# Kernel tuning notes

Measured on AMD Instinct MI355X. Metric: run time of the kernel, lower is better.

The kernel has to match this reference:

```python
import jax, jax.numpy as jnp
import numpy as np

EPS = 1e-5  # BatchNorm eps (torch default)

def setup_inputs() -> dict:
    key = jax.random.key(0)
    ks = jax.random.split(key, 24)
    B, NX, NY, F = 8, 128, 128, 128
    dims = [2 * F, 512, 256, 128, 64]
    d = {
        'x': jax.random.normal(ks[0], (B, NX, F), dtype=jnp.float32),
        'y': jax.random.normal(ks[1], (B, NY, F), dtype=jnp.float32),
    }
    i = 2
    for li, (din, dout) in enumerate(zip(dims[:-1], dims[1:]), start=1):
        d[f'w{li}'] = jax.random.normal(ks[i], (dout, din), dtype=jnp.float32) * (1.0 / np.sqrt(din)); i += 1
        d[f'b{li}'] = jax.random.normal(ks[i], (dout,), dtype=jnp.float32) * 0.02; i += 1
        if li < 4:  # BatchNorm1d on hidden layers only (eval mode: running stats)
            d[f'g{li}'] = 1.0 + 0.1 * jax.random.normal(ks[i], (dout,), dtype=jnp.float32); i += 1
            d[f'be{li}'] = 0.1 * jax.random.normal(ks[i], (dout,), dtype=jnp.float32); i += 1
            d[f'm{li}'] = 0.1 * jax.random.normal(ks[i], (dout,), dtype=jnp.float32); i += 1
            d[f'v{li}'] = 0.5 + jax.random.uniform(ks[i], (dout,), dtype=jnp.float32); i += 1
    return d

def _bn(h, g, be, m, v):
    # BatchNorm1d in eval mode over the channel (last) axis
    return (h - m) * (g * jax.lax.rsqrt(v + EPS)) + be

def reference(x, y,
              w1, b1, g1, be1, m1, v1,
              w2, b2, g2, be2, m2, v2,
              w3, b3, g3, be3, m3, v3,
              w4, b4):
    F = x.shape[-1]
    # First Linear on cat([x_i, y_j]) == split-weight broadcast add: avoids the
    # (B,nx,ny,2F) pairwise concat the torch code materializes (same math).
    wx, wy = w1[:, :F], w1[:, F:]                      # (512,F) each
    hx = jnp.einsum('bif,hf->bih', x, wx)              # (B,nx,512)
    hy = jnp.einsum('bjf,hf->bjh', y, wy)              # (B,ny,512)
    h = hx[:, :, None, :] + hy[:, None, :, :] + b1     # (B,nx,ny,512)
    h = jax.nn.relu(_bn(h, g1, be1, m1, v1))           # dropout is identity in eval
    h = jax.nn.relu(_bn(jnp.einsum('bijh,oh->bijo', h, w2) + b2, g2, be2, m2, v2))
    h = jax.nn.relu(_bn(jnp.einsum('bijh,oh->bijo', h, w3) + b3, g3, be3, m3, v3))
    e = jnp.einsum('bijh,oh->bijo', h, w4) + b4        # (B,nx,ny,64) embeddings
    # PSD path: einsum('bijk,bilk->bijl', e, e).sum(-1)
    #         == sum_k e[b,i,j,k] * (sum_l e[b,i,l,k])  -- avoids (B,nx,ny,ny)
    s = e.sum(axis=2)                                  # (B,nx,64)
    kernel = jnp.einsum('bijk,bik->bij', e, s)         # (B,nx,ny)
    return kernel
```

## Files before the change

kernel.cpp:

```cpp
#include <hip/hip_runtime.h>

#define EPS 1e-5f

typedef _Float16 half8 __attribute__((ext_vector_type(8)));
typedef _Float16 half4 __attribute__((ext_vector_type(4)));
typedef float f32x16 __attribute__((ext_vector_type(16)));
typedef float f32x4v __attribute__((ext_vector_type(4)));


__global__ __launch_bounds__(256)
void pre_kernel(
    const float* __restrict__ x, const float* __restrict__ y,
    const float* __restrict__ w1, const float* __restrict__ b1,
    const float* __restrict__ g1, const float* __restrict__ be1,
    const float* __restrict__ m1, const float* __restrict__ v1,
    const float* __restrict__ w2, const float* __restrict__ b2,
    const float* __restrict__ g2, const float* __restrict__ be2,
    const float* __restrict__ m2, const float* __restrict__ v2,
    const float* __restrict__ w3, const float* __restrict__ b3,
    const float* __restrict__ g3, const float* __restrict__ be3,
    const float* __restrict__ m3, const float* __restrict__ v3,
    const float* __restrict__ w4,
    _Float16* __restrict__ hxh, _Float16* __restrict__ hyh,
    _Float16* __restrict__ w2h, _Float16* __restrict__ w3h,
    _Float16* __restrict__ w4h,
    float* __restrict__ b2f, float* __restrict__ b3f)
{
    const int t = threadIdx.x;

    if (blockIdx.x >= 256) {
        int tid = (blockIdx.x - 256) * 256 + t;
        const int nth = 64 * 256;
        for (int idx = tid; idx < 256 * 512; idx += nth) {
            int n = idx >> 9, k = idx & 511;
            float a = g2[n] * rsqrtf(v2[n] + EPS);
            int addr = ((n >> 5) * 32 + (k >> 4)) * 512 + ((k >> 3) & 1) * 256 + (n & 31) * 8 + (k & 7);
            w2h[addr] = (_Float16)(a * w2[idx]);
        }
        for (int idx = tid; idx < 128 * 256; idx += nth) {
            int n = idx >> 8, k = idx & 255;
            float a = g3[n] * rsqrtf(v3[n] + EPS);
            int addr = ((n >> 5) * 16 + (k >> 4)) * 512 + ((k >> 3) & 1) * 256 + (n & 31) * 8 + (k & 7);
            w3h[addr] = (_Float16)(a * w3[idx]);
        }
        for (int idx = tid; idx < 64 * 128; idx += nth) {
            int n = idx >> 7, k = idx & 127;
            int addr = ((n >> 5) * 8 + (k >> 4)) * 512 + ((k >> 3) & 1) * 256 + (n & 31) * 8 + (k & 7);
            w4h[addr] = (_Float16)w4[idx];
        }
        if (tid < 256) {
            float a = g2[tid] * rsqrtf(v2[tid] + EPS);
            b2f[tid] = a * b2[tid] + be2[tid] - m2[tid] * a;
        } else if (tid < 384) {
            int n = tid - 256;
            float a = g3[n] * rsqrtf(v3[n] + EPS);
            b3f[n] = a * b3[n] + be3[n] - m3[n] * a;
        }
        return;
    }

    const int rg = blockIdx.x & 31;
    const int ng = (blockIdx.x >> 5) & 3;
    const int which = blockIdx.x >> 7;

    constexpr int LDA = 136;
    __shared__ _Float16 sh[32 * 136 + 128 * 136] __attribute__((aligned(16)));
    _Float16* xa = sh;
    _Float16* wb = sh + 32 * 136;

    const int rowbase = rg * 32;
    const float* src = which ? y : x;

#pragma unroll
    for (int p = 0; p < 4; ++p) {
        int c = p * 256 + t;
        int r = c >> 5, fo = (c & 31) * 4;
        f32x4v v = *(const f32x4v*)(src + (size_t)(rowbase + r) * 128 + fo);
        half4 h; h[0] = (_Float16)v[0]; h[1] = (_Float16)v[1];
        h[2] = (_Float16)v[2]; h[3] = (_Float16)v[3];
        *(half4*)(xa + r * LDA + fo) = h;
    }
#pragma unroll
    for (int p = 0; p < 16; ++p) {
        int c = p * 256 + t;
        int n = c >> 5, fo = (c & 31) * 4;
        f32x4v v = *(const f32x4v*)(w1 + (size_t)(ng * 128 + n) * 256 + which * 128 + fo);
        half4 h; h[0] = (_Float16)v[0]; h[1] = (_Float16)v[1];
        h[2] = (_Float16)v[2]; h[3] = (_Float16)v[3];
        *(half4*)(wb + n * LDA + fo) = h;
    }
    __syncthreads();

    const int wid = t >> 6;
    const int l = t & 63;
    const int l31 = l & 31, lh = l >> 5;

    f32x16 acc = (f32x16)0.f;
#pragma unroll
    for (int kc = 0; kc < 8; ++kc) {
        half8 af = *(const half8*)(xa + l31 * LDA + kc * 16 + lh * 8);
        half8 bf = *(const half8*)(wb + (wid * 32 + l31) * LDA + kc * 16 + lh * 8);
        acc = __builtin_amdgcn_mfma_f32_32x32x16_f16(af, bf, acc, 0, 0, 0);
    }

    const int n = ng * 128 + wid * 32 + l31;
    float alpha = g1[n] * rsqrtf(v1[n] + EPS);
    if (which == 0) {
        float bias = alpha * b1[n] + be1[n] - m1[n] * alpha;
#pragma unroll
        for (int r = 0; r < 16; ++r) {
            int m = (r & 3) + 8 * (r >> 2) + 4 * lh;
            hxh[(size_t)(rowbase + m) * 512 + n] = (_Float16)(alpha * acc[r] + bias);
        }
    } else {
        const int ks = n >> 4, lhh = (n >> 3) & 1, c = n & 7;
#pragma unroll
        for (int r = 0; r < 16; ++r) {
            int m = (r & 3) + 8 * (r >> 2) + 4 * lh;
            int R = rowbase + m;
            int bb = R >> 7, j = R & 127;
            int addr = bb * 65536 + ((j >> 5) * 32 + ks) * 512 + lhh * 256 + (j & 31) * 8 + c;
            hyh[addr] = (_Float16)(alpha * acc[r]);
        }
    }
}

__global__ __launch_bounds__(1024, 4)
void fused_kernel(
    const _Float16* __restrict__ hxh, const _Float16* __restrict__ hyh,
    const _Float16* __restrict__ w2h, const _Float16* __restrict__ w3h,
    const _Float16* __restrict__ w4h,
    const float* __restrict__ b2f, const float* __restrict__ b3f,
    const float* __restrict__ b4,
    float* __restrict__ out)
{
    constexpr int LD2 = 264;
    constexpr int LD3 = 136;
    constexpr int LDE = 68;
    constexpr int REG = 67584;

    __shared__ char smem[8192 + 2 * REG] __attribute__((aligned(16)));
    _Float16* hxs = (_Float16*)smem;
    float* spart  = (float*)(smem + 2048);
    float* ss     = (float*)(smem + 6144);
    char* R1 = smem + 8192;
    _Float16* a1 = (_Float16*)R1;

    const int b  = blockIdx.x >> 6;
    const int ip = blockIdx.x & 63;
    const int i0 = ip * 2;
    const int t = threadIdx.x;
    const int wid = t >> 6;
    const int l   = t & 63;
    const int l31 = l & 31;
    const int lh  = l >> 5;

    if (t < 128) {
        int iv = t >> 6;
        *(half8*)(hxs + iv * 512 + (t & 63) * 8) =
            *(const half8*)(hxh + (size_t)(b * 128 + i0 + iv) * 512 + (t & 63) * 8);
    }
    __syncthreads();

    const int srg = wid >> 2, sksl = wid & 3;
    const _Float16* hysrc = hyh + (size_t)b * 65536
                          + (size_t)(srg * 32 + sksl) * 512 + l * 8;
    const int wm = wid >> 2, wn = wid & 3;
    const _Float16* pb0 = w2h + (size_t)(2 * wn) * 32 * 512 + l * 8;
    const _Float16* pb1 = pb0 + 32 * 512;

    const float bb0 = b2f[wn * 64 + l31];
    const float bb1 = b2f[wn * 64 + 32 + l31];
    f32x16 d0 = (f32x16)bb0, d1 = (f32x16)bb1;
    f32x16 e0 = (f32x16)bb0, e1 = (f32x16)bb1;

    half8 hyreg;

    auto SLOAD = [&](int c) {
        hyreg = *(const half8*)(hysrc + (size_t)c * 4 * 512);
    };
    auto SFIN = [&](int c) {
        const int ksg = c * 4 + sksl;
        half8 hx0 = *(const half8*)(hxs + ksg * 16 + lh * 8);
        half8 hx1 = *(const half8*)(hxs + 512 + ksg * 16 + lh * 8);
        half8 s0 = hyreg + hx0;
        half8 s1 = hyreg + hx1;
        half8 a0, a1f;
#pragma unroll
        for (int cc = 0; cc < 8; ++cc) {
            a0[cc]  = s0[cc] > (_Float16)0.f ? s0[cc] : (_Float16)0.f;
            a1f[cc] = s1[cc] > (_Float16)0.f ? s1[cc] : (_Float16)0.f;
        }
        _Float16* dst = a1 + (size_t)((c & 1) * 32 + srg * 4 + sksl) * 512 + l * 8;
        *(half8*)dst = a0;
        *(half8*)(dst + 16 * 512) = a1f;
    };
    auto CONSUME = [&](int c) {
        const _Float16* ab0 = a1 + (size_t)((c & 1) * 32 + wm * 4) * 512 + l * 8;
        const _Float16* ab1 = ab0 + 16 * 512;
#pragma unroll
        for (int ksl = 0; ksl < 4; ++ksl) {
            const int ksg = c * 4 + ksl;
            half8 Ai0 = *(const half8*)(ab0 + ksl * 512);
            half8 Ai1 = *(const half8*)(ab1 + ksl * 512);
            half8 Bx  = *(const half8*)(pb0 + (size_t)ksg * 512);
            half8 By  = *(const half8*)(pb1 + (size_t)ksg * 512);
            d0 = __builtin_amdgcn_mfma_f32_32x32x16_f16(Ai0, Bx, d0, 0, 0, 0);
            d1 = __builtin_amdgcn_mfma_f32_32x32x16_f16(Ai0, By, d1, 0, 0, 0);
            e0 = __builtin_amdgcn_mfma_f32_32x32x16_f16(Ai1, Bx, e0, 0, 0, 0);
            e1 = __builtin_amdgcn_mfma_f32_32x32x16_f16(Ai1, By, e1, 0, 0, 0);
        }
    };

    SLOAD(0);
    SFIN(0);
    __syncthreads();
#pragma unroll 2
    for (int c = 0; c < 8; ++c) {
        if (c < 7) SLOAD(c + 1);
        CONSUME(c);
        if (c < 7) SFIN(c + 1);
        __syncthreads();
    }

    {
        _Float16* a2_0 = (_Float16*)R1;
        _Float16* a2_1 = (_Float16*)(R1 + REG);
#pragma unroll
        for (int r = 0; r < 16; ++r) {
            int m = wm * 32 + (r & 3) + 8 * (r >> 2) + 4 * lh;
            a2_0[m * LD2 + wn * 64 + l31]      = (_Float16)fmaxf(d0[r], 0.f);
            a2_0[m * LD2 + wn * 64 + 32 + l31] = (_Float16)fmaxf(d1[r], 0.f);
            a2_1[m * LD2 + wn * 64 + l31]      = (_Float16)fmaxf(e0[r], 0.f);
            a2_1[m * LD2 + wn * 64 + 32 + l31] = (_Float16)fmaxf(e1[r], 0.f);
        }
    }
    __syncthreads();

    const int team = wid >> 3;
    const int tw   = wid & 7;
    char* reg = R1 + team * REG;
    _Float16* a2 = (_Float16*)reg;
    _Float16* a3 = (_Float16*)reg;
    float*    es = (float*)reg;
    float* spart_t = spart + team * 512;
    float* ss_t    = ss + team * 64;
    const int iv = i0 + team;

    const int wm3 = tw >> 2, wn3 = tw & 3;
    f32x16 g0, g1;
    {
        float b3v = b3f[wn3 * 32 + l31];
        g0 = (f32x16)b3v;
        g1 = (f32x16)b3v;
    }
#pragma unroll 4
    for (int kc = 0; kc < 16; ++kc) {
        half8 bfr = *(const half8*)(w3h + (wn3 * 16 + kc) * 512 + l * 8);
        half8 af0 = *(const half8*)(a2 + (wm3 * 64 + l31) * LD2 + kc * 16 + lh * 8);
        half8 af1 = *(const half8*)(a2 + (wm3 * 64 + 32 + l31) * LD2 + kc * 16 + lh * 8);
        g0 = __builtin_amdgcn_mfma_f32_32x32x16_f16(af0, bfr, g0, 0, 0, 0);
        g1 = __builtin_amdgcn_mfma_f32_32x32x16_f16(af1, bfr, g1, 0, 0, 0);
    }
    __syncthreads();
#pragma unroll
    for (int mt = 0; mt < 2; ++mt)
#pragma unroll
        for (int r = 0; r < 16; ++r) {
            int m = wm3 * 64 + mt * 32 + (r & 3) + 8 * (r >> 2) + 4 * lh;
            a3[m * LD3 + wn3 * 32 + l31] = (_Float16)fmaxf(mt ? g1[r] : g0[r], 0.f);
        }
    __syncthreads();

    const int wm4 = tw >> 1, wn4 = tw & 1;
    f32x16 acc4 = (f32x16)(b4[wn4 * 32 + l31]);
#pragma unroll
    for (int kc = 0; kc < 8; ++kc) {
        half8 afr = *(const half8*)(a3 + (wm4 * 32 + l31) * LD3 + kc * 16 + lh * 8);
        half8 bfr = *(const half8*)(w4h + (wn4 * 8 + kc) * 512 + l * 8);
        acc4 = __builtin_amdgcn_mfma_f32_32x32x16_f16(afr, bfr, acc4, 0, 0, 0);
    }
    __syncthreads();
#pragma unroll
    for (int r = 0; r < 16; ++r) {
        int m = wm4 * 32 + (r & 3) + 8 * (r >> 2) + 4 * lh;
        es[m * LDE + wn4 * 32 + l31] = acc4[r];
    }
    __syncthreads();

    {
        float sv = 0.f;
#pragma unroll
        for (int jj = 0; jj < 16; ++jj) sv += es[(tw + jj * 8) * LDE + l];
        spart_t[tw * 64 + l] = sv;
    }
    __syncthreads();
    if ((t & 511) < 64) {
        int tt = t & 63;
        float s2 = 0.f;
#pragma unroll
        for (int r = 0; r < 8; ++r) s2 += spart_t[r * 64 + tt];
        ss_t[tt] = s2;
    }
    __syncthreads();
    {
        const int tt = t & 511;
        const int j = tt >> 2, q = tt & 3;
        float p = 0.f;
#pragma unroll
        for (int c = 0; c < 16; ++c) {
            int k = q + 4 * c;
            p += es[j * LDE + k] * ss_t[k];
        }
        p += __shfl_xor(p, 1);
        p += __shfl_xor(p, 2);
        if (q == 0) out[(size_t)(b * 128 + iv) * 128 + j] = p;
    }
}

extern "C" void kernel_launch(void* const* d_in, const int* in_sizes, int n_in,
                              void* d_out, int out_size, void* d_ws, size_t ws_size,
                              hipStream_t stream)
{
    (void)in_sizes; (void)n_in; (void)out_size; (void)ws_size;

    const float* x   = (const float*)d_in[0];
    const float* y   = (const float*)d_in[1];
    const float* w1  = (const float*)d_in[2];
    const float* b1  = (const float*)d_in[3];
    const float* g1  = (const float*)d_in[4];
    const float* be1 = (const float*)d_in[5];
    const float* m1  = (const float*)d_in[6];
    const float* v1  = (const float*)d_in[7];
    const float* w2  = (const float*)d_in[8];
    const float* b2  = (const float*)d_in[9];
    const float* g2  = (const float*)d_in[10];
    const float* be2 = (const float*)d_in[11];
    const float* m2  = (const float*)d_in[12];
    const float* v2  = (const float*)d_in[13];
    const float* w3  = (const float*)d_in[14];
    const float* b3  = (const float*)d_in[15];
    const float* g3  = (const float*)d_in[16];
    const float* be3 = (const float*)d_in[17];
    const float* m3  = (const float*)d_in[18];
    const float* v3  = (const float*)d_in[19];
    const float* w4  = (const float*)d_in[20];
    const float* b4  = (const float*)d_in[21];
    float* out = (float*)d_out;

    float* b2f = (float*)d_ws;
    float* b3f = b2f + 256;
    _Float16* w2h = (_Float16*)(b3f + 128);
    _Float16* w3h = w2h + 131072;
    _Float16* w4h = w3h + 32768;
    _Float16* hxh = w4h + 8192;
    _Float16* hyh = hxh + 524288;

    hipLaunchKernelGGL(pre_kernel, dim3(320), dim3(256), 0, stream,
                       x, y, w1, b1, g1, be1, m1, v1,
                       w2, b2, g2, be2, m2, v2,
                       w3, b3, g3, be3, m3, v3,
                       w4,
                       hxh, hyh, w2h, w3h, w4h, b2f, b3f);

    hipLaunchKernelGGL(fused_kernel, dim3(512), dim3(1024), 0, stream,
                       hxh, hyh, w2h, w3h, w4h, b2f, b3f, b4, out);
}
```

Baseline: 63.37 us.

## Transpose MFMA operand roles so weights are A and activations B with vectorized epilogues

Swaps the MFMA operand roles in layers 2-4 so weights feed the A operand and activations feed B. The accumulator rows then map to output channels, which lets each lane write four contiguous halves or floats per store and apply bias through vector loads in the epilogue, instead of scattering single elements. It also regroups the layer-2 K pipeline into 4 chunks of 8 k-slices, halving the barrier count, with each wave staging two slices per chunk. The cost is a different LDS staging layout, more registers held per wave, and bias now added in the epilogue rather than used to seed the accumulators.

```diff
diff --git a/kernel.cpp b/kernel.cpp
--- a/kernel.cpp
+++ b/kernel.cpp
@@ -162,77 +162,89 @@
     }
     __syncthreads();
 
-    const int srg = wid >> 2, sksl = wid & 3;
-    const _Float16* hysrc = hyh + (size_t)b * 65536
-                          + (size_t)(srg * 32 + sksl) * 512 + l * 8;
-    const int wm = wid >> 2, wn = wid & 3;
-    const _Float16* pb0 = w2h + (size_t)(2 * wn) * 32 * 512 + l * 8;
-    const _Float16* pb1 = pb0 + 32 * 512;
-
-    const float bb0 = b2f[wn * 64 + l31];
-    const float bb1 = b2f[wn * 64 + 32 + l31];
-    f32x16 d0 = (f32x16)bb0, d1 = (f32x16)bb1;
-    f32x16 e0 = (f32x16)bb0, e1 = (f32x16)bb1;
-
-    half8 hyreg;
+    const int u = wid >> 2, v = wid & 3;
+    const int sk2 = (v) * 2;
+    const _Float16* hysrc = hyh + (size_t)b * 65536 + (size_t)u * 32 * 512 + l * 8;
+    const _Float16* pa0 = w2h + (size_t)(2 * u) * 32 * 512 + l * 8;
+    const _Float16* pa1 = pa0 + 32 * 512;
+
+    f32x16 d0 = (f32x16)0.f, d1 = (f32x16)0.f;
+    f32x16 e0 = (f32x16)0.f, e1 = (f32x16)0.f;
+
+    half8 hyr0, hyr1;
 
     auto SLOAD = [&](int c) {
-        hyreg = *(const half8*)(hysrc + (size_t)c * 4 * 512);
+        hyr0 = *(const half8*)(hysrc + (size_t)(c * 8 + sk2) * 512);
+        hyr1 = *(const half8*)(hysrc + (size_t)(c * 8 + sk2 + 1) * 512);
     };
     auto SFIN = [&](int c) {
-        const int ksg = c * 4 + sksl;
-        half8 hx0 = *(const half8*)(hxs + ksg * 16 + lh * 8);
-        half8 hx1 = *(const half8*)(hxs + 512 + ksg * 16 + lh * 8);
-        half8 s0 = hyreg + hx0;
-        half8 s1 = hyreg + hx1;
-        half8 a0, a1f;
-#pragma unroll
-        for (int cc = 0; cc < 8; ++cc) {
-            a0[cc]  = s0[cc] > (_Float16)0.f ? s0[cc] : (_Float16)0.f;
-            a1f[cc] = s1[cc] > (_Float16)0.f ? s1[cc] : (_Float16)0.f;
-        }
-        _Float16* dst = a1 + (size_t)((c & 1) * 32 + srg * 4 + sksl) * 512 + l * 8;
-        *(half8*)dst = a0;
-        *(half8*)(dst + 16 * 512) = a1f;
+#pragma unroll
+        for (int kk = 0; kk < 2; ++kk) {
+            const int ksl = sk2 + kk;
+            const int ksg = c * 8 + ksl;
+            half8 hy = kk ? hyr1 : hyr0;
+            half8 hx0 = *(const half8*)(hxs + ksg * 16 + lh * 8);
+            half8 hx1 = *(const half8*)(hxs + 512 + ksg * 16 + lh * 8);
+            half8 s0 = hy + hx0;
+            half8 s1 = hy + hx1;
+            half8 a0, a1f;
+#pragma unroll
+            for (int cc = 0; cc < 8; ++cc) {
+                a0[cc]  = s0[cc] > (_Float16)0.f ? s0[cc] : (_Float16)0.f;
+                a1f[cc] = s1[cc] > (_Float16)0.f ? s1[cc] : (_Float16)0.f;
+            }
+            _Float16* dst = a1 + (size_t)((c & 1) * 64 + u * 8 + ksl) * 512 + l * 8;
+            *(half8*)dst = a0;
+            *(half8*)(dst + 32 * 512) = a1f;
+        }
     };
     auto CONSUME = [&](int c) {
-        const _Float16* ab0 = a1 + (size_t)((c & 1) * 32 + wm * 4) * 512 + l * 8;
-        const _Float16* ab1 = ab0 + 16 * 512;
-#pragma unroll
-        for (int ksl = 0; ksl < 4; ++ksl) {
-            const int ksg = c * 4 + ksl;
-            half8 Ai0 = *(const half8*)(ab0 + ksl * 512);
-            half8 Ai1 = *(const half8*)(ab1 + ksl * 512);
-            half8 Bx  = *(const half8*)(pb0 + (size_t)ksg * 512);
-            half8 By  = *(const half8*)(pb1 + (size_t)ksg * 512);
-            d0 = __builtin_amdgcn_mfma_f32_32x32x16_f16(Ai0, Bx, d0, 0, 0, 0);
-            d1 = __builtin_amdgcn_mfma_f32_32x32x16_f16(Ai0, By, d1, 0, 0, 0);
-            e0 = __builtin_amdgcn_mfma_f32_32x32x16_f16(Ai1, Bx, e0, 0, 0, 0);
-            e1 = __builtin_amdgcn_mfma_f32_32x32x16_f16(Ai1, By, e1, 0, 0, 0);
+#pragma unroll 4
+        for (int ksl = 0; ksl < 8; ++ksl) {
+            const _Float16* bsl = a1 + (size_t)((c & 1) * 64 + v * 8 + ksl) * 512 + l * 8;
+            half8 Bi0 = *(const half8*)bsl;
+            half8 Bi1 = *(const half8*)(bsl + 32 * 512);
+            half8 A0 = *(const half8*)(pa0 + (size_t)(c * 8 + ksl) * 512);
+            half8 A1 = *(const half8*)(pa1 + (size_t)(c * 8 + ksl) * 512);
+            d0 = __builtin_amdgcn_mfma_f32_32x32x16_f16(A0, Bi0, d0, 0, 0, 0);
+            d1 = __builtin_amdgcn_mfma_f32_32x32x16_f16(A1, Bi0, d1, 0, 0, 0);
+            e0 = __builtin_amdgcn_mfma_f32_32x32x16_f16(A0, Bi1, e0, 0, 0, 0);
+            e1 = __builtin_amdgcn_mfma_f32_32x32x16_f16(A1, Bi1, e1, 0, 0, 0);
         }
     };
 
     SLOAD(0);
     SFIN(0);
     __syncthreads();
-#pragma unroll 2
-    for (int c = 0; c < 8; ++c) {
-        if (c < 7) SLOAD(c + 1);
+    for (int c = 0; c < 4; ++c) {
+        if (c < 3) SLOAD(c + 1);
         CONSUME(c);
-        if (c < 7) SFIN(c + 1);
+        if (c < 3) SFIN(c + 1);
         __syncthreads();
     }
 
     {
         _Float16* a2_0 = (_Float16*)R1;
         _Float16* a2_1 = (_Float16*)(R1 + REG);
-#pragma unroll
-        for (int r = 0; r < 16; ++r) {
-            int m = wm * 32 + (r & 3) + 8 * (r >> 2) + 4 * lh;
-            a2_0[m * LD2 + wn * 64 + l31]      = (_Float16)fmaxf(d0[r], 0.f);
-            a2_0[m * LD2 + wn * 64 + 32 + l31] = (_Float16)fmaxf(d1[r], 0.f);
-            a2_1[m * LD2 + wn * 64 + l31]      = (_Float16)fmaxf(e0[r], 0.f);
-            a2_1[m * LD2 + wn * 64 + 32 + l31] = (_Float16)fmaxf(e1[r], 0.f);
+        const int j2 = v * 32 + l31;
+#pragma unroll
+        for (int g = 0; g < 2; ++g) {
+            const f32x16 cd = g ? d1 : d0;
+            const f32x16 ce = g ? e1 : e0;
+            const int ngb = (2 * u + g) * 32;
+#pragma unroll
+            for (int q = 0; q < 4; ++q) {
+                const int no = ngb + 8 * q + 4 * lh;
+                f32x4v bv = *(const f32x4v*)(b2f + no);
+                half4 h0, h1;
+#pragma unroll
+                for (int cc = 0; cc < 4; ++cc) {
+                    h0[cc] = (_Float16)fmaxf(cd[4 * q + cc] + bv[cc], 0.f);
+                    h1[cc] = (_Float16)fmaxf(ce[4 * q + cc] + bv[cc], 0.f);
+                }
+                *(half4*)(a2_0 + j2 * LD2 + no) = h0;
+                *(half4*)(a2_1 + j2 * LD2 + no) = h1;
+            }
         }
     }
     __syncthreads();
@@ -247,44 +259,56 @@
     float* ss_t    = ss + team * 64;
     const int iv = i0 + team;
 
-    const int wm3 = tw >> 2, wn3 = tw & 3;
-    f32x16 g0, g1;
-    {
-        float b3v = b3f[wn3 * 32 + l31];
-        g0 = (f32x16)b3v;
-        g1 = (f32x16)b3v;
-    }
+    const int uo = tw >> 2, vj = tw & 3;
+    const int j3 = vj * 32 + l31;
+    f32x16 g0 = (f32x16)0.f, g1 = (f32x16)0.f;
 #pragma unroll 4
     for (int kc = 0; kc < 16; ++kc) {
-        half8 bfr = *(const half8*)(w3h + (wn3 * 16 + kc) * 512 + l * 8);
-        half8 af0 = *(const half8*)(a2 + (wm3 * 64 + l31) * LD2 + kc * 16 + lh * 8);
-        half8 af1 = *(const half8*)(a2 + (wm3 * 64 + 32 + l31) * LD2 + kc * 16 + lh * 8);
-        g0 = __builtin_amdgcn_mfma_f32_32x32x16_f16(af0, bfr, g0, 0, 0, 0);
-        g1 = __builtin_amdgcn_mfma_f32_32x32x16_f16(af1, bfr, g1, 0, 0, 0);
-    }
-    __syncthreads();
-#pragma unroll
-    for (int mt = 0; mt < 2; ++mt)
-#pragma unroll
-        for (int r = 0; r < 16; ++r) {
-            int m = wm3 * 64 + mt * 32 + (r & 3) + 8 * (r >> 2) + 4 * lh;
-            a3[m * LD3 + wn3 * 32 + l31] = (_Float16)fmaxf(mt ? g1[r] : g0[r], 0.f);
-        }
-    __syncthreads();
-
-    const int wm4 = tw >> 1, wn4 = tw & 1;
-    f32x16 acc4 = (f32x16)(b4[wn4 * 32 + l31]);
+        half8 A0 = *(const half8*)(w3h + ((2 * uo) * 16 + kc) * 512 + l * 8);
+        half8 A1 = *(const half8*)(w3h + ((2 * uo + 1) * 16 + kc) * 512 + l * 8);
+        half8 Bf = *(const half8*)(a2 + j3 * LD2 + kc * 16 + lh * 8);
+        g0 = __builtin_amdgcn_mfma_f32_32x32x16_f16(A0, Bf, g0, 0, 0, 0);
+        g1 = __builtin_amdgcn_mfma_f32_32x32x16_f16(A1, Bf, g1, 0, 0, 0);
+    }
+    __syncthreads();
+    {
+#pragma unroll
+        for (int g = 0; g < 2; ++g) {
+            const f32x16 cg = g ? g1 : g0;
+            const int ogb = (2 * uo + g) * 32;
+#pragma unroll
+            for (int q = 0; q < 4; ++q) {
+                const int oo = ogb + 8 * q + 4 * lh;
+                f32x4v bv = *(const f32x4v*)(b3f + oo);
+                half4 h;
+#pragma unroll
+                for (int cc = 0; cc < 4; ++cc)
+                    h[cc] = (_Float16)fmaxf(cg[4 * q + cc] + bv[cc], 0.f);
+                *(half4*)(a3 + j3 * LD3 + oo) = h;
+            }
+        }
+    }
+    __syncthreads();
+
+    const int up = tw >> 2;
+    f32x16 a4 = (f32x16)0.f;
 #pragma unroll
     for (int kc = 0; kc < 8; ++kc) {
-        half8 afr = *(const half8*)(a3 + (wm4 * 32 + l31) * LD3 + kc * 16 + lh * 8);
-        half8 bfr = *(const half8*)(w4h + (wn4 * 8 + kc) * 512 + l * 8);
-        acc4 = __builtin_amdgcn_mfma_f32_32x32x16_f16(afr, bfr, acc4, 0, 0, 0);
-    }
-    __syncthreads();
-#pragma unroll
-    for (int r = 0; r < 16; ++r) {
-        int m = wm4 * 32 + (r & 3) + 8 * (r >> 2) + 4 * lh;
-        es[m * LDE + wn4 * 32 + l31] = acc4[r];
+        half8 A = *(const half8*)(w4h + (up * 8 + kc) * 512 + l * 8);
+        half8 B = *(const half8*)(a3 + j3 * LD3 + kc * 16 + lh * 8);
+        a4 = __builtin_amdgcn_mfma_f32_32x32x16_f16(A, B, a4, 0, 0, 0);
+    }
+    __syncthreads();
+    {
+#pragma unroll
+        for (int q = 0; q < 4; ++q) {
+            const int pp = up * 32 + 8 * q + 4 * lh;
+            f32x4v bv = *(const f32x4v*)(b4 + pp);
+            f32x4v vv;
+#pragma unroll
+            for (int cc = 0; cc < 4; ++cc) vv[cc] = a4[4 * q + cc] + bv[cc];
+            *(f32x4v*)(es + j3 * LDE + pp) = vv;
+        }
     }
     __syncthreads();
 
```

Measured after the change: 68.63 us. +8.3%, slower.
